# Optimization experiments

Measured on AMD Instinct MI355X. Metric: run time of the kernel, lower is better.

The kernel has to match this reference:

```python
import jax, jax.numpy as jnp
import numpy as np

B, C, H, W = 4, 16, 320, 640


def _propagate_front(x, g):
    """Linear propagation along leading axis.
    x, g: [L, ...]. out[0] = x[0]; out[i] = x[i]*(1-g[i]) + g[i]*out[i-1].
    """
    def step(prev, xg):
        xr, gr = xg
        out = xr * (1.0 - gr) + gr * prev
        return out, out
    _, ys = jax.lax.scan(step, x[0], (x[1:], g[1:]))
    return jnp.concatenate([x[:1], ys], axis=0)


def _propagate(x, g, axis, reverse):
    xm = jnp.moveaxis(x, axis, 0)
    gm = jnp.moveaxis(g, axis, 0)
    if reverse:
        xm = xm[::-1]
        gm = gm[::-1]
    ym = _propagate_front(xm, gm)
    if reverse:
        ym = ym[::-1]
    return jnp.moveaxis(ym, 0, axis)


def setup_inputs() -> dict:
    key = jax.random.key(0)
    ks = jax.random.split(key, 5)
    shape = (B, C, H, W)
    return {
        "input": jax.random.normal(ks[0], shape, dtype=jnp.float32),
        "g0": jax.random.uniform(ks[1], shape, dtype=jnp.float32),
        "g1": jax.random.uniform(ks[2], shape, dtype=jnp.float32),
        "g2": jax.random.uniform(ks[3], shape, dtype=jnp.float32),
        "g3": jax.random.uniform(ks[4], shape, dtype=jnp.float32),
    }


def reference(input, g0, g1, g2, g3):
    # 4-directional gated recurrent grid propagation, fused by elementwise max.
    r_down = _propagate(input, g0, axis=2, reverse=False)   # top -> bottom over H
    r_up = _propagate(input, g1, axis=2, reverse=True)      # bottom -> top over H
    r_right = _propagate(input, g2, axis=3, reverse=False)  # left -> right over W
    r_left = _propagate(input, g3, axis=3, reverse=True)    # right -> left over W
    return jnp.maximum(jnp.maximum(jnp.maximum(r_down, r_up), r_right), r_left)
```

## Files before the change

kernel.cpp:

```cpp
#include <hip/hip_runtime.h>

constexpr int Bn = 4;
constexpr int Cn = 16;
constexpr int Hn = 320;
constexpr int Wn = 640;
constexpr int NCOL = Bn * Cn * Wn;
constexpr int NROW = Bn * Cn * Hn;

constexpr int HS = 10;
constexpr int NS = 32;
constexpr int CPB = 32;
constexpr int GPW = Wn / CPB;

#define REP10(M) M(0) M(1) M(2) M(3) M(4) M(5) M(6) M(7) M(8) M(9)
#define REP10R(M) M(9) M(8) M(7) M(6) M(5) M(4) M(3) M(2) M(1) M(0)

__global__ __launch_bounds__(1024, 2) void vert_both(
    const float* __restrict__ x, const float* __restrict__ g0,
    const float* __restrict__ g1, float* __restrict__ vm) {
  __shared__ float As[NS][CPB], Bs[NS][CPB];
  __shared__ float dstash[NS][HS][CPB];
  const int grp = blockIdx.x;
  const int bc = grp / GPW;
  const int w0 = (grp % GPW) * CPB;
  const int s = threadIdx.x >> 5;
  const int l = threadIdx.x & 31;
  const int colbase = bc * (Hn * Wn) + w0 + l;
  const int base = colbase + (s * HS) * Wn;

#define DECLD(i) float rd##i, pd##i;
  REP10(DECLD)
#undef DECLD
  {
    int off = base;
    float yy = 0.0f, pp = 1.0f;
#define DSTEP(i)                                                      \
    {                                                                 \
      float xv = x[off];                                              \
      float gv = g0[off];                                             \
      float bb = (s == 0 && i == 0) ? 0.0f : gv;                      \
      yy = fmaf(bb, yy - xv, xv);                                     \
      pp *= bb;                                                       \
      rd##i = yy;                                                     \
      pd##i = pp;                                                     \
      off += Wn;                                                      \
    }
    REP10(DSTEP)
#undef DSTEP
    As[s][l] = yy;
    Bs[s][l] = pp;
  }
  __syncthreads();
  if (s == 0) {
    float c = 0.0f;
#pragma unroll
    for (int ss = 0; ss < NS; ++ss) {
      float a = As[ss][l], b = Bs[ss][l];
      As[ss][l] = c;
      c = fmaf(b, c, a);
    }
  }
  __syncthreads();

  {
    const float cd = As[s][l];
#define STASH(i) dstash[s][i][l] = fmaf(pd##i, cd, rd##i);
    REP10(STASH)
#undef STASH
  }
  __syncthreads();

#define DECLU(i) float yu##i, pu##i;
  REP10(DECLU)
#undef DECLU
  {
    int off = base + (HS - 1) * Wn;
    float yy = 0.0f, pp = 1.0f;
#define USTEP(i)                                                      \
    {                                                                 \
      float xv = x[off];                                              \
      float gv = g1[off];                                             \
      float bb = (s == NS - 1 && i == HS - 1) ? 0.0f : gv;            \
      yy = fmaf(bb, yy - xv, xv);                                     \
      pp *= bb;                                                       \
      yu##i = yy;                                                     \
      pu##i = pp;                                                     \
      off -= Wn;                                                      \
    }
    REP10R(USTEP)
#undef USTEP
    As[s][l] = yy;
    Bs[s][l] = pp;
  }
  __syncthreads();
  if (s == 0) {
    float c = 0.0f;
#pragma unroll
    for (int ss = NS - 1; ss >= 0; --ss) {
      float a = As[ss][l], b = Bs[ss][l];
      As[ss][l] = c;
      c = fmaf(b, c, a);
    }
  }
  __syncthreads();

  {
    const float cu = As[s][l];
    int off = base + (HS - 1) * Wn;
#define FSTEP(i)                                                      \
    {                                                                 \
      float u = fmaf(pu##i, cu, yu##i);                               \
      vm[off] = fmaxf(dstash[s][i][l], u);                            \
      off -= Wn;                                                      \
    }
    REP10R(FSTEP)
#undef FSTEP
  }
}

constexpr int WSEG = 10;

__global__ __launch_bounds__(256) void horiz_final(
    const float* __restrict__ x, const float* __restrict__ g2,
    const float* __restrict__ g3, const float* __restrict__ vm,
    float* __restrict__ out) {
  __shared__ float xs[4 * Wn], rrs[4 * Wn], rls[4 * Wn];
  const int tid = threadIdx.x, wv = tid >> 6, l = tid & 63;
  const size_t rowbase = (size_t)blockIdx.x * 4 * Wn;

  const float4* xg = (const float4*)(x + rowbase);
  const float4* g2g = (const float4*)(g2 + rowbase);
  const float4* g3g = (const float4*)(g3 + rowbase);
  const float4* vm4 = (const float4*)(vm + rowbase);
  float4* xsv = (float4*)xs;
  float4* rrv = (float4*)rrs;
  float4* rlv = (float4*)rls;

  const int i0 = tid, i1 = tid + 256, i2 = tid + 512;
  float4 v0, v1, v2;
  xsv[i0] = xg[i0]; rrv[i0] = g2g[i0]; rlv[i0] = g3g[i0]; v0 = vm4[i0];
  xsv[i1] = xg[i1]; rrv[i1] = g2g[i1]; rlv[i1] = g3g[i1]; v1 = vm4[i1];
  if (i2 < Wn) { xsv[i2] = xg[i2]; rrv[i2] = g2g[i2]; rlv[i2] = g3g[i2]; v2 = vm4[i2]; }
  __syncthreads();

  const int rb = wv * Wn + l * WSEG;
  float xl[WSEG], gl[WSEG], yl[WSEG], pl[WSEG];
#pragma unroll
  for (int i = 0; i < WSEG; ++i) { xl[i] = xs[rb + i]; gl[i] = rrs[rb + i]; }

  {
    float y = 0.0f, p = 1.0f;
#pragma unroll
    for (int i = 0; i < WSEG; ++i) {
      float bb = (l == 0 && i == 0) ? 0.0f : gl[i];
      y = fmaf(bb, y - xl[i], xl[i]);
      p *= bb;
      yl[i] = y; pl[i] = p;
    }
    float A = y, B = p;
#pragma unroll
    for (int off = 1; off < 64; off <<= 1) {
      float Au = __shfl_up(A, off);
      float Bu = __shfl_up(B, off);
      if (l >= off) { A = fmaf(B, Au, A); B *= Bu; }
    }
    float c = __shfl_up(A, 1);
    if (l == 0) c = 0.0f;
#pragma unroll
    for (int i = 0; i < WSEG; ++i) rrs[rb + i] = fmaf(pl[i], c, yl[i]);
  }

#pragma unroll
  for (int i = 0; i < WSEG; ++i) gl[i] = rls[rb + i];
  {
    float y = 0.0f, p = 1.0f;
#pragma unroll
    for (int i = WSEG - 1; i >= 0; --i) {
      float bb = (l == 63 && i == WSEG - 1) ? 0.0f : gl[i];
      y = fmaf(bb, y - xl[i], xl[i]);
      p *= bb;
      yl[i] = y; pl[i] = p;
    }
    float A = y, B = p;
#pragma unroll
    for (int off = 1; off < 64; off <<= 1) {
      float Ad = __shfl_down(A, off);
      float Bd = __shfl_down(B, off);
      if (l + off < 64) { A = fmaf(B, Ad, A); B *= Bd; }
    }
    float c = __shfl_down(A, 1);
    if (l == 63) c = 0.0f;
#pragma unroll
    for (int i = 0; i < WSEG; ++i) rls[rb + i] = fmaf(pl[i], c, yl[i]);
  }
  __syncthreads();

  float4* o4 = (float4*)(out + rowbase);
  {
    float4 a = rrv[i0], b = rlv[i0];
    float4 o;
    o.x = fmaxf(fmaxf(a.x, b.x), v0.x);
    o.y = fmaxf(fmaxf(a.y, b.y), v0.y);
    o.z = fmaxf(fmaxf(a.z, b.z), v0.z);
    o.w = fmaxf(fmaxf(a.w, b.w), v0.w);
    o4[i0] = o;
  }
  {
    float4 a = rrv[i1], b = rlv[i1];
    float4 o;
    o.x = fmaxf(fmaxf(a.x, b.x), v1.x);
    o.y = fmaxf(fmaxf(a.y, b.y), v1.y);
    o.z = fmaxf(fmaxf(a.z, b.z), v1.z);
    o.w = fmaxf(fmaxf(a.w, b.w), v1.w);
    o4[i1] = o;
  }
  if (i2 < Wn) {
    float4 a = rrv[i2], b = rlv[i2];
    float4 o;
    o.x = fmaxf(fmaxf(a.x, b.x), v2.x);
    o.y = fmaxf(fmaxf(a.y, b.y), v2.y);
    o.z = fmaxf(fmaxf(a.z, b.z), v2.z);
    o.w = fmaxf(fmaxf(a.w, b.w), v2.w);
    o4[i2] = o;
  }
}

extern "C" void kernel_launch(void* const* d_in, const int* in_sizes, int n_in,
                              void* d_out, int out_size, void* d_ws,
                              size_t ws_size, hipStream_t stream) {
  const float* x = (const float*)d_in[0];
  const float* g0 = (const float*)d_in[1];
  const float* g1 = (const float*)d_in[2];
  const float* g2 = (const float*)d_in[3];
  const float* g3 = (const float*)d_in[4];
  float* out = (float*)d_out;

  vert_both<<<NCOL / CPB, 1024, 0, stream>>>(x, g0, g1, out);
  horiz_final<<<NROW / 4, 256, 0, stream>>>(x, g2, g3, out, out);
}
```

Before: 262.1 us.

## Vectorize vertical scan with float4 columns and keep down results in registers

The vertical kernel now gives each thread four adjacent columns as float4, so each block covers 128 columns with wider global loads and stores. The down-scan results stay in registers instead of a shared-memory stash, and the synchronization around that stash is removed. Occupancy is pinned with amdgpu_waves_per_eu(4,4). The cost is much higher register pressure from holding 80 float4 values per thread, which risks spilling, and each block now covers four times as many columns.

```diff
diff --git a/kernel.cpp b/kernel.cpp
--- a/kernel.cpp
+++ b/kernel.cpp
@@ -9,111 +9,138 @@
 
 constexpr int HS = 10;
 constexpr int NS = 32;
-constexpr int CPB = 32;
+constexpr int TC = 32;
+constexpr int CPB = TC * 4;
 constexpr int GPW = Wn / CPB;
+constexpr int W4 = Wn / 4;
 
 #define REP10(M) M(0) M(1) M(2) M(3) M(4) M(5) M(6) M(7) M(8) M(9)
 #define REP10R(M) M(9) M(8) M(7) M(6) M(5) M(4) M(3) M(2) M(1) M(0)
 
-__global__ __launch_bounds__(1024, 2) void vert_both(
+#define SCAN4(gv, xv, yy, pp)                                         \
+  yy.x = fmaf(gv.x, yy.x - xv.x, xv.x); pp.x *= gv.x;                 \
+  yy.y = fmaf(gv.y, yy.y - xv.y, xv.y); pp.y *= gv.y;                 \
+  yy.z = fmaf(gv.z, yy.z - xv.z, xv.z); pp.z *= gv.z;                 \
+  yy.w = fmaf(gv.w, yy.w - xv.w, xv.w); pp.w *= gv.w;
+
+__global__ __launch_bounds__(1024)
+__attribute__((amdgpu_waves_per_eu(4, 4))) void vert_both(
     const float* __restrict__ x, const float* __restrict__ g0,
     const float* __restrict__ g1, float* __restrict__ vm) {
-  __shared__ float As[NS][CPB], Bs[NS][CPB];
-  __shared__ float dstash[NS][HS][CPB];
+  __shared__ float4 As[NS][TC], Bs[NS][TC];
   const int grp = blockIdx.x;
   const int bc = grp / GPW;
-  const int w0 = (grp % GPW) * CPB;
+  const int q0 = (grp % GPW) * TC;
   const int s = threadIdx.x >> 5;
-  const int l = threadIdx.x & 31;
-  const int colbase = bc * (Hn * Wn) + w0 + l;
-  const int base = colbase + (s * HS) * Wn;
-
-#define DECLD(i) float rd##i, pd##i;
+  const int tc = threadIdx.x & 31;
+  const int base = bc * (Hn * W4) + (s * HS) * W4 + q0 + tc;
+  const float4* x4 = (const float4*)x;
+  const float4* g04 = (const float4*)g0;
+  const float4* g14 = (const float4*)g1;
+  float4* vm4 = (float4*)vm;
+
+#define DECLD(i) float4 rd##i, pd##i;
   REP10(DECLD)
 #undef DECLD
+
   {
     int off = base;
-    float yy = 0.0f, pp = 1.0f;
+    float4 yy = make_float4(0.f, 0.f, 0.f, 0.f);
+    float4 pp = make_float4(1.f, 1.f, 1.f, 1.f);
 #define DSTEP(i)                                                      \
     {                                                                 \
-      float xv = x[off];                                              \
-      float gv = g0[off];                                             \
-      float bb = (s == 0 && i == 0) ? 0.0f : gv;                      \
-      yy = fmaf(bb, yy - xv, xv);                                     \
-      pp *= bb;                                                       \
+      float4 xv = x4[off];                                            \
+      float4 gv = g04[off];                                           \
+      if (s == 0 && i == 0) gv = make_float4(0.f, 0.f, 0.f, 0.f);     \
+      SCAN4(gv, xv, yy, pp)                                           \
       rd##i = yy;                                                     \
       pd##i = pp;                                                     \
-      off += Wn;                                                      \
+      off += W4;                                                      \
     }
     REP10(DSTEP)
 #undef DSTEP
-    As[s][l] = yy;
-    Bs[s][l] = pp;
-  }
-  __syncthreads();
-  if (s == 0) {
-    float c = 0.0f;
+    As[s][tc] = yy;
+    Bs[s][tc] = pp;
+  }
+  __syncthreads();
+  if (threadIdx.x < 32) {
+    const int t = threadIdx.x;
+    float4 c = make_float4(0.f, 0.f, 0.f, 0.f);
 #pragma unroll
     for (int ss = 0; ss < NS; ++ss) {
-      float a = As[ss][l], b = Bs[ss][l];
-      As[ss][l] = c;
-      c = fmaf(b, c, a);
-    }
-  }
-  __syncthreads();
-
-  {
-    const float cd = As[s][l];
-#define STASH(i) dstash[s][i][l] = fmaf(pd##i, cd, rd##i);
-    REP10(STASH)
-#undef STASH
-  }
-  __syncthreads();
-
-#define DECLU(i) float yu##i, pu##i;
+      float4 a = As[ss][t], b = Bs[ss][t];
+      As[ss][t] = c;
+      c.x = fmaf(b.x, c.x, a.x);
+      c.y = fmaf(b.y, c.y, a.y);
+      c.z = fmaf(b.z, c.z, a.z);
+      c.w = fmaf(b.w, c.w, a.w);
+    }
+  }
+  __syncthreads();
+
+  {
+    const float4 cd = As[s][tc];
+#define FIXD(i)                                                       \
+    rd##i.x = fmaf(pd##i.x, cd.x, rd##i.x);                           \
+    rd##i.y = fmaf(pd##i.y, cd.y, rd##i.y);                           \
+    rd##i.z = fmaf(pd##i.z, cd.z, rd##i.z);                           \
+    rd##i.w = fmaf(pd##i.w, cd.w, rd##i.w);
+    REP10(FIXD)
+#undef FIXD
+  }
+
+#define DECLU(i) float4 yu##i, pu##i;
   REP10(DECLU)
 #undef DECLU
   {
-    int off = base + (HS - 1) * Wn;
-    float yy = 0.0f, pp = 1.0f;
+    int off = base + (HS - 1) * W4;
+    float4 yy = make_float4(0.f, 0.f, 0.f, 0.f);
+    float4 pp = make_float4(1.f, 1.f, 1.f, 1.f);
 #define USTEP(i)                                                      \
     {                                                                 \
-      float xv = x[off];                                              \
-      float gv = g1[off];                                             \
-      float bb = (s == NS - 1 && i == HS - 1) ? 0.0f : gv;            \
-      yy = fmaf(bb, yy - xv, xv);                                     \
-      pp *= bb;                                                       \
+      float4 xv = x4[off];                                            \
+      float4 gv = g14[off];                                           \
+      if (s == NS - 1 && i == HS - 1) gv = make_float4(0.f, 0.f, 0.f, 0.f); \
+      SCAN4(gv, xv, yy, pp)                                           \
       yu##i = yy;                                                     \
       pu##i = pp;                                                     \
-      off -= Wn;                                                      \
+      off -= W4;                                                      \
     }
     REP10R(USTEP)
 #undef USTEP
-    As[s][l] = yy;
-    Bs[s][l] = pp;
-  }
-  __syncthreads();
-  if (s == 0) {
-    float c = 0.0f;
+    As[s][tc] = yy;
+    Bs[s][tc] = pp;
+  }
+  __syncthreads();
+  if (threadIdx.x < 32) {
+    const int t = threadIdx.x;
+    float4 c = make_float4(0.f, 0.f, 0.f, 0.f);
 #pragma unroll
     for (int ss = NS - 1; ss >= 0; --ss) {
-      float a = As[ss][l], b = Bs[ss][l];
-      As[ss][l] = c;
-      c = fmaf(b, c, a);
-    }
-  }
-  __syncthreads();
-
-  {
-    const float cu = As[s][l];
-    int off = base + (HS - 1) * Wn;
+      float4 a = As[ss][t], b = Bs[ss][t];
+      As[ss][t] = c;
+      c.x = fmaf(b.x, c.x, a.x);
+      c.y = fmaf(b.y, c.y, a.y);
+      c.z = fmaf(b.z, c.z, a.z);
+      c.w = fmaf(b.w, c.w, a.w);
+    }
+  }
+  __syncthreads();
+
+  {
+    const float4 cu = As[s][tc];
+    int off = base;
 #define FSTEP(i)                                                      \
     {                                                                 \
-      float u = fmaf(pu##i, cu, yu##i);                               \
-      vm[off] = fmaxf(dstash[s][i][l], u);                            \
-      off -= Wn;                                                      \
-    }
-    REP10R(FSTEP)
+      float4 o;                                                       \
+      o.x = fmaxf(rd##i.x, fmaf(pu##i.x, cu.x, yu##i.x));             \
+      o.y = fmaxf(rd##i.y, fmaf(pu##i.y, cu.y, yu##i.y));             \
+      o.z = fmaxf(rd##i.z, fmaf(pu##i.z, cu.z, yu##i.z));             \
+      o.w = fmaxf(rd##i.w, fmaf(pu##i.w, cu.w, yu##i.w));             \
+      vm4[off] = o;                                                   \
+      off += W4;                                                      \
+    }
+    REP10(FSTEP)
 #undef FSTEP
   }
 }
```

Result: slower. 321.5 us (+22.7%).
